# Kernel tuning notes

Measured on AMD Instinct MI355X. Metric: run time of the kernel, lower is better.

The kernel has to match this reference:

```python
import jax, jax.numpy as jnp
import numpy as np

H_IMG, W_IMG = 32, 32   # image_size -> seq_len = 1024
NH, HD, D = 8, 32, 256  # num_heads, head_dim, d_model
B = 8


def _relative_positions(h, w):
    # Swin-style relative position index table, [h*w, h*w] int32
    y = np.arange(h); x = np.arange(w)
    coords = np.stack(np.meshgrid(y, x, indexing='ij')).reshape(2, -1)  # [2, S]
    rel = coords[:, :, None] - coords[:, None, :]                      # [2, S, S]
    rel = rel.transpose(1, 2, 0).astype(np.int64)                      # [S, S, 2]
    rel[:, :, 0] += h - 1
    rel[:, :, 1] += w - 1
    rel[:, :, 0] *= 2 * w - 1
    return np.int32(rel.sum(-1))                                       # [S, S]

_POS = _relative_positions(H_IMG, W_IMG)


def setup_inputs() -> dict:
    key = jax.random.key(0)
    ks = jax.random.split(key, 8)
    S = H_IMG * W_IMG
    return {
        'inputs_q': jax.random.normal(ks[0], (B, S, D), jnp.float32),
        'inputs_kv': jax.random.normal(ks[1], (B, S, D), jnp.float32),
        'Wq': jax.random.normal(ks[2], (D, NH, HD), jnp.float32) / np.sqrt(D),
        'bq': jnp.zeros((NH, HD), jnp.float32),
        'Wk': jax.random.normal(ks[3], (D, NH, HD), jnp.float32) / np.sqrt(D),
        'bk': jnp.zeros((NH, HD), jnp.float32),
        'Wv': jax.random.normal(ks[4], (D, NH, HD), jnp.float32) / np.sqrt(D),
        'bv': jnp.zeros((NH, HD), jnp.float32),
        'rel_table': 0.02 * jax.random.normal(ks[5], ((2 * H_IMG - 1) * (2 * W_IMG - 1), NH), jnp.float32),
        'Wo': jax.random.normal(ks[6], (NH, HD, D), jnp.float32) / np.sqrt(NH * HD),
        'bo': jnp.zeros((D,), jnp.float32),
    }


def reference(inputs_q, inputs_kv, Wq, bq, Wk, bk, Wv, bv, rel_table, Wo, bo):
    pos = jnp.asarray(_POS)                                  # [S, S] int32 (constant)
    q = jnp.einsum('bsd,dhk->bshk', inputs_q, Wq) + bq       # [B, S, H, HD]
    k = jnp.einsum('bsd,dhk->bshk', inputs_kv, Wk) + bk
    v = jnp.einsum('bsd,dhk->bshk', inputs_kv, Wv) + bv
    q = q / jnp.sqrt(jnp.asarray(HD, q.dtype))
    attn = jnp.einsum('bqhd,bkhd->bhqk', q, k)               # [B, H, S, S]
    rel_bias = rel_table[pos]                                # [S, S, H]
    attn = attn + jnp.transpose(rel_bias, (2, 0, 1))[None]   # broadcast over batch
    attn = jax.nn.softmax(attn, axis=-1)
    x = jnp.einsum('bhqk,bkhd->bqhd', attn, v)               # [B, S, H, HD]
    return jnp.einsum('bqhd,hdf->bqf', x, Wo) + bo           # [B, S, D]
```

## Files before the change

kernel.cpp:

```cpp
#include <hip/hip_runtime.h>

#define B_SZ   8
#define S_LEN  1024
#define D_MOD  256
#define NHEADS 8
#define M_ROWS 8192
#define LOG2E  1.4426950408889634f
#define QSCALE_LOG2E 0.2550352766751165f

typedef _Float16 f16x8 __attribute__((ext_vector_type(8)));
typedef _Float16 f16x4 __attribute__((ext_vector_type(4)));
typedef float    f32x4 __attribute__((ext_vector_type(4)));

__global__ __launch_bounds__(256)
void prep_kernel(const float* __restrict__ Wq, const float* __restrict__ Wk,
                 const float* __restrict__ Wv, const float* __restrict__ Wo,
                 const float* __restrict__ rel,
                 _Float16* __restrict__ wtp, float* __restrict__ tab) {
    if (blockIdx.x < 32) {
        __shared__ _Float16 Wl[32 * 264];
        const int mi = blockIdx.x >> 3;
        const int k0 = (blockIdx.x & 7) << 5;
        const float* W = (mi == 0) ? Wq : (mi == 1) ? Wk : (mi == 2) ? Wv : Wo;
        {
            const int r  = threadIdx.x >> 3;
            const int c4 = (threadIdx.x & 7) * 4;
            const float* src = W + (size_t)(k0 + r) * 256 + c4;
#pragma unroll
            for (int g = 0; g < 8; ++g) {
                f32x4 v = *(const f32x4*)(src + g * 32);
                f16x4 o;
#pragma unroll
                for (int j = 0; j < 4; ++j) o[j] = (_Float16)v[j];
                *(f16x4*)(&Wl[r * 264 + c4 + g * 32]) = o;
            }
        }
        __syncthreads();
        const int n16 = threadIdx.x >> 4;
        const int l16 = threadIdx.x & 15;
        const int kk  = k0 >> 5;
#pragma unroll
        for (int quad = 0; quad < 4; ++quad) {
            f16x8 v;
#pragma unroll
            for (int j = 0; j < 8; ++j) v[j] = Wl[(quad * 8 + j) * 264 + n16 * 16 + l16];
            *(f16x8*)(wtp + (((size_t)(mi * 16 + n16) * 8 + kk) << 9) + (quad * 16 + l16) * 8) = v;
        }
        return;
    }
    __shared__ float rl[63 * 8];
    const int dy31 = blockIdx.x - 32;
    for (int f = threadIdx.x; f < 504; f += 256) rl[f] = rel[(size_t)dy31 * 504 + f];
    __syncthreads();
    const int h  = threadIdx.x >> 5;
    const int r5 = threadIdx.x & 31;
#pragma unroll
    for (int c = 0; c < 6; ++c) {
        const int oi   = r5 * 6 + c;
        const int e    = oi >> 6;
        const int lane = oi & 63;
        const int quad = lane >> 4, l16 = lane & 15;
        f32x4 v;
#pragma unroll
        for (int reg = 0; reg < 4; ++reg) {
            const int idx = 16 * e + l16 - quad * 4 - reg + 15;
            v[reg] = rl[idx * 8 + h] * LOG2E;
        }
        *(f32x4*)(tab + (((size_t)(h * 63 + dy31) * 3 + e) << 8) + lane * 4) = v;
    }
}

__global__ __launch_bounds__(256)
void gemm_qkv_kernel(const float* __restrict__ in_q, const float* __restrict__ in_kv,
                     const _Float16* __restrict__ wtp,
                     const float* __restrict__ bq, const float* __restrict__ bk,
                     const float* __restrict__ bv,
                     _Float16* __restrict__ qs, _Float16* __restrict__ ks,
                     _Float16* __restrict__ vs) {
    __shared__ __align__(16) _Float16 As[64 * 264];
    _Float16* Ta = As;
    _Float16* Tb = As + 64 * 72;

    const int tid  = threadIdx.x;
    const int w    = tid >> 6;
    const int lane = tid & 63;
    const int quad = lane >> 4;
    const int l16  = lane & 15;
    const int m0 = blockIdx.x * 64, n0 = blockIdx.y * 64, z = blockIdx.z;
    const int b = m0 >> 10, mloc = m0 & 1023;

    {
        const int r  = tid >> 2;
        const int c4 = (tid & 3) * 4;
        const float* src = (z ? in_kv : in_q) + (size_t)(m0 + r) * 256 + c4;
        _Float16* dst = As + r * 264 + c4;
#pragma unroll
        for (int g = 0; g < 16; ++g) {
            f32x4 v = *(const f32x4*)(src + g * 16);
            f16x4 o;
#pragma unroll
            for (int j = 0; j < 4; ++j) o[j] = (_Float16)v[j];
            *(f16x4*)(dst + g * 16) = o;
        }
    }
    __syncthreads();

    const int n16base = (n0 >> 4) + (w >> 1) * 2;
    const int mA = z ? 1 : 0;
    const _Float16* wA0 = wtp + (((size_t)(mA * 16 + n16base + 0) * 8) << 9) + lane * 8;
    const _Float16* wA1 = wtp + (((size_t)(mA * 16 + n16base + 1) * 8) << 9) + lane * 8;
    const _Float16* wV0 = wtp + (((size_t)(2 * 16 + n16base + 0) * 8) << 9) + lane * 8;
    const _Float16* wV1 = wtp + (((size_t)(2 * 16 + n16base + 1) * 8) << 9) + lane * 8;
    const _Float16* arow0 = As + ((w & 1) * 32 + l16) * 264;
    const _Float16* arow1 = arow0 + 16 * 264;

    f32x4 accA[2][2], accV[2][2];
#pragma unroll
    for (int i = 0; i < 2; ++i)
#pragma unroll
        for (int j = 0; j < 2; ++j) {
            accA[i][j] = (f32x4){0.f, 0.f, 0.f, 0.f};
            accV[i][j] = (f32x4){0.f, 0.f, 0.f, 0.f};
        }

#pragma unroll
    for (int kk = 0; kk < 8; ++kk) {
        const int k8 = kk * 32 + quad * 8;
        f16x8 a0 = *(const f16x8*)(arow0 + k8);
        f16x8 a1 = *(const f16x8*)(arow1 + k8);
        f16x8 w0 = *(const f16x8*)(wA0 + kk * 512);
        f16x8 w1 = *(const f16x8*)(wA1 + kk * 512);
        accA[0][0] = __builtin_amdgcn_mfma_f32_16x16x32_f16(w0, a0, accA[0][0], 0, 0, 0);
        accA[0][1] = __builtin_amdgcn_mfma_f32_16x16x32_f16(w0, a1, accA[0][1], 0, 0, 0);
        accA[1][0] = __builtin_amdgcn_mfma_f32_16x16x32_f16(w1, a0, accA[1][0], 0, 0, 0);
        accA[1][1] = __builtin_amdgcn_mfma_f32_16x16x32_f16(w1, a1, accA[1][1], 0, 0, 0);
        if (z == 1) {
            f16x8 v0 = *(const f16x8*)(wV0 + kk * 512);
            f16x8 v1 = *(const f16x8*)(wV1 + kk * 512);
            accV[0][0] = __builtin_amdgcn_mfma_f32_16x16x32_f16(a0, v0, accV[0][0], 0, 0, 0);
            accV[0][1] = __builtin_amdgcn_mfma_f32_16x16x32_f16(a0, v1, accV[0][1], 0, 0, 0);
            accV[1][0] = __builtin_amdgcn_mfma_f32_16x16x32_f16(a1, v0, accV[1][0], 0, 0, 0);
            accV[1][1] = __builtin_amdgcn_mfma_f32_16x16x32_f16(a1, v1, accV[1][1], 0, 0, 0);
        }
    }
    __syncthreads();

    {
        const float* biasA = z ? bk : bq;
        const float  sc    = z ? 1.0f : QSCALE_LOG2E;
#pragma unroll
        for (int i = 0; i < 2; ++i) {
            f32x4 b4 = *(const f32x4*)(biasA + n0 + (w >> 1) * 32 + i * 16 + quad * 4);
#pragma unroll
            for (int jj = 0; jj < 2; ++jj) {
                f16x4 pk;
#pragma unroll
                for (int r = 0; r < 4; ++r) pk[r] = (_Float16)((accA[i][jj][r] + b4[r]) * sc);
                *(f16x4*)(Ta + ((w & 1) * 32 + jj * 16 + l16) * 72 +
                               (w >> 1) * 32 + i * 16 + quad * 4) = pk;
            }
        }
        if (z == 1) {
#pragma unroll
            for (int i = 0; i < 2; ++i) {
                const float bvv = bv[n0 + (w >> 1) * 32 + i * 16 + l16];
#pragma unroll
                for (int jj = 0; jj < 2; ++jj) {
                    f16x4 pk;
#pragma unroll
                    for (int r = 0; r < 4; ++r) pk[r] = (_Float16)(accV[jj][i][r] + bvv);
                    *(f16x4*)(Tb + ((w >> 1) * 32 + i * 16 + l16) * 72 +
                                   (w & 1) * 32 + jj * 16 + quad * 4) = pk;
                }
            }
        }
    }
    __syncthreads();
    {
        const int l16c = tid & 15, qdc = (tid >> 4) & 3;
        const int tile0 = mloc >> 5;
#pragma unroll
        for (int c2i = 0; c2i < 2; ++c2i) {
            const int c2 = w * 2 + c2i;
            const int s2 = c2 >> 2, sub = (c2 >> 1) & 1, hs = c2 & 1;
            const int bh = b * 8 + (n0 >> 5) + hs;
            const size_t dbase = (((size_t)(bh * 32 + tile0 + s2) * 2 + sub) << 9) + lane * 8;
            f16x8 va = *(const f16x8*)(Ta + (s2 * 32 + sub * 16 + l16c) * 72 +
                                            hs * 32 + qdc * 8);
            *(f16x8*)((z ? ks : qs) + dbase) = va;
            if (z == 1) {
                f16x8 vb = *(const f16x8*)(Tb + (hs * 32 + sub * 16 + l16c) * 72 +
                                                s2 * 32 + qdc * 8);
                *(f16x8*)(vs + dbase) = vb;
            }
        }
    }
}

__global__ __launch_bounds__(256)
void gemm_out_kernel(const _Float16* __restrict__ xh, const _Float16* __restrict__ wtp,
                     const float* __restrict__ bo, float* __restrict__ out) {
    __shared__ __align__(16) _Float16 As[64 * 264];
    const int tid  = threadIdx.x;
    const int w    = tid >> 6;
    const int lane = tid & 63;
    const int quad = lane >> 4;
    const int l16  = lane & 15;
    const int m0 = blockIdx.x * 64, n0 = blockIdx.y * 64;

    {
        const int r  = tid >> 2;
        const int c8 = (tid & 3) * 8;
        const _Float16* src = xh + (size_t)(m0 + r) * 256 + c8;
        _Float16* dst = As + r * 264 + c8;
#pragma unroll
        for (int g = 0; g < 8; ++g)
            *(f16x8*)(dst + g * 32) = *(const f16x8*)(src + g * 32);
    }
    __syncthreads();

    const int n16base = 48 + (n0 >> 4) + (w >> 1) * 2;
    const _Float16* w0p = wtp + (((size_t)(n16base + 0) * 8) << 9) + lane * 8;
    const _Float16* w1p = wtp + (((size_t)(n16base + 1) * 8) << 9) + lane * 8;
    const _Float16* arow0 = As + ((w & 1) * 32 + l16) * 264;
    const _Float16* arow1 = arow0 + 16 * 264;

    f32x4 acc[2][2];
#pragma unroll
    for (int i = 0; i < 2; ++i)
#pragma unroll
        for (int j = 0; j < 2; ++j) acc[i][j] = (f32x4){0.f, 0.f, 0.f, 0.f};

#pragma unroll
    for (int kk = 0; kk < 8; ++kk) {
        const int k8 = kk * 32 + quad * 8;
        f16x8 a0 = *(const f16x8*)(arow0 + k8);
        f16x8 a1 = *(const f16x8*)(arow1 + k8);
        f16x8 b0 = *(const f16x8*)(w0p + kk * 512);
        f16x8 b1 = *(const f16x8*)(w1p + kk * 512);
        acc[0][0] = __builtin_amdgcn_mfma_f32_16x16x32_f16(a0, b0, acc[0][0], 0, 0, 0);
        acc[0][1] = __builtin_amdgcn_mfma_f32_16x16x32_f16(a0, b1, acc[0][1], 0, 0, 0);
        acc[1][0] = __builtin_amdgcn_mfma_f32_16x16x32_f16(a1, b0, acc[1][0], 0, 0, 0);
        acc[1][1] = __builtin_amdgcn_mfma_f32_16x16x32_f16(a1, b1, acc[1][1], 0, 0, 0);
    }

    __syncthreads();
    {
        float* Tf = (float*)As;
#pragma unroll
        for (int i = 0; i < 2; ++i) {
#pragma unroll
            for (int jj = 0; jj < 2; ++jj) {
#pragma unroll
                for (int r = 0; r < 4; ++r) {
                    const int row = (w & 1) * 32 + jj * 16 + quad * 4 + r;
                    const int col = (w >> 1) * 32 + i * 16 + l16;
                    Tf[row * 68 + col] = acc[jj][i][r];
                }
            }
        }
        __syncthreads();
        const f32x4 bv4 = *(const f32x4*)(bo + n0 + l16 * 4);
#pragma unroll
        for (int g = 0; g < 4; ++g) {
            const int row = w * 16 + g * 4 + quad;
            f32x4 v = *(const f32x4*)(Tf + row * 68 + l16 * 4);
            v += bv4;
            *(f32x4*)(out + (size_t)(m0 + row) * 256 + n0 + l16 * 4) = v;
        }
    }
}

__global__ __launch_bounds__(256)
void attn_kernel(const _Float16* __restrict__ qs, const _Float16* __restrict__ ks,
                 const _Float16* __restrict__ vs, const float* __restrict__ tab,
                 _Float16* __restrict__ xh) {
    __shared__ __align__(16) _Float16 Ps[4][32][40];

    const int tid  = threadIdx.x;
    const int w    = tid >> 6;
    const int lane = tid & 63;
    const int quad = lane >> 4;
    const int l16  = lane & 15;

    const int n     = blockIdx.x;
    const int xcd   = n & 7;
    const int local = n >> 3;
    const int bh    = xcd * 8 + (local & 7);
    const int qc    = local >> 3;
    const int b = bh >> 3, h = bh & 7;
    const int qrow_base = qc * 128 + w * 32;
    const int yq = qc * 4 + w;

    const _Float16* qp = qs + (((size_t)(bh * 32 + yq) * 2) << 9) + lane * 8;
    const f16x8 qf0 = *(const f16x8*)(qp);
    const f16x8 qf1 = *(const f16x8*)(qp + 512);
    const _Float16* kp = ks + (((size_t)bh * 64) << 9) + lane * 8;
    const _Float16* vp = vs + (((size_t)bh * 64) << 9) + lane * 8;
    const float* tb = tab + (((size_t)h * 63 * 3) << 8) + lane * 4;

    f16x8 ones;
#pragma unroll
    for (int j = 0; j < 8; ++j) ones[j] = (_Float16)1.0f;

    f32x4 o00 = {0.f,0.f,0.f,0.f}, o01 = {0.f,0.f,0.f,0.f};
    f32x4 o10 = {0.f,0.f,0.f,0.f}, o11 = {0.f,0.f,0.f,0.f};
    f32x4 ol0 = {0.f,0.f,0.f,0.f}, ol1 = {0.f,0.f,0.f,0.f};

    f16x8 kf0 = *(const f16x8*)(kp);
    f16x8 kf1 = *(const f16x8*)(kp + 512);
    f16x8 vf0 = *(const f16x8*)(vp);
    f16x8 vf1 = *(const f16x8*)(vp + 512);
    f32x4 c0 = *(const f32x4*)(tb + (yq + 31) * 768);
    f32x4 c1 = *(const f32x4*)(tb + (yq + 31) * 768 + 256);
    f32x4 c2 = *(const f32x4*)(tb + (yq + 31) * 768 + 512);

    for (int kt = 0; kt < 32; ++kt) {
        const bool more = (kt < 31);
        f16x8 nk0, nk1, nv0, nv1;
        f32x4 nc0, nc1, nc2;
        if (more) {
            const _Float16* kq = kp + (kt + 1) * 1024;
            nk0 = *(const f16x8*)(kq);
            nk1 = *(const f16x8*)(kq + 512);
            const _Float16* vq = vp + (kt + 1) * 1024;
            nv0 = *(const f16x8*)(vq);
            nv1 = *(const f16x8*)(vq + 512);
            const int d = (yq + 30 - kt) * 768;
            nc0 = *(const f32x4*)(tb + d);
            nc1 = *(const f32x4*)(tb + d + 256);
            nc2 = *(const f32x4*)(tb + d + 512);
        }

        __builtin_amdgcn_s_setprio(1);
        f32x4 s00 = __builtin_amdgcn_mfma_f32_16x16x32_f16(kf0, qf0, c1, 0, 0, 0);
        f32x4 s01 = __builtin_amdgcn_mfma_f32_16x16x32_f16(kf1, qf0, c0, 0, 0, 0);
        f32x4 s10 = __builtin_amdgcn_mfma_f32_16x16x32_f16(kf0, qf1, c2, 0, 0, 0);
        f32x4 s11 = __builtin_amdgcn_mfma_f32_16x16x32_f16(kf1, qf1, c1, 0, 0, 0);
        __builtin_amdgcn_s_setprio(0);

        f16x4 p;
#pragma unroll
        for (int r = 0; r < 4; ++r) p[r] = (_Float16)__builtin_amdgcn_exp2f(s00[r]);
        *(f16x4*)(&Ps[w][l16][quad * 4]) = p;
#pragma unroll
        for (int r = 0; r < 4; ++r) p[r] = (_Float16)__builtin_amdgcn_exp2f(s01[r]);
        *(f16x4*)(&Ps[w][l16][16 + quad * 4]) = p;
#pragma unroll
        for (int r = 0; r < 4; ++r) p[r] = (_Float16)__builtin_amdgcn_exp2f(s10[r]);
        *(f16x4*)(&Ps[w][16 + l16][quad * 4]) = p;
#pragma unroll
        for (int r = 0; r < 4; ++r) p[r] = (_Float16)__builtin_amdgcn_exp2f(s11[r]);
        *(f16x4*)(&Ps[w][16 + l16][16 + quad * 4]) = p;

        const f16x8 pf0 = *(const f16x8*)(&Ps[w][l16][quad * 8]);
        const f16x8 pf1 = *(const f16x8*)(&Ps[w][16 + l16][quad * 8]);
        __builtin_amdgcn_s_setprio(1);
        o00 = __builtin_amdgcn_mfma_f32_16x16x32_f16(vf0, pf0, o00, 0, 0, 0);
        o01 = __builtin_amdgcn_mfma_f32_16x16x32_f16(vf0, pf1, o01, 0, 0, 0);
        o10 = __builtin_amdgcn_mfma_f32_16x16x32_f16(vf1, pf0, o10, 0, 0, 0);
        o11 = __builtin_amdgcn_mfma_f32_16x16x32_f16(vf1, pf1, o11, 0, 0, 0);
        ol0 = __builtin_amdgcn_mfma_f32_16x16x32_f16(ones, pf0, ol0, 0, 0, 0);
        ol1 = __builtin_amdgcn_mfma_f32_16x16x32_f16(ones, pf1, ol1, 0, 0, 0);
        __builtin_amdgcn_s_setprio(0);

        if (more) {
            kf0 = nk0; kf1 = nk1; vf0 = nv0; vf1 = nv1;
            c0 = nc0; c1 = nc1; c2 = nc2;
        }
    }

#pragma unroll
    for (int qh = 0; qh < 2; ++qh) {
        const f32x4 onl = qh ? o01 : o00;
        const f32x4 onh = qh ? o11 : o10;
        const f32x4 ll  = qh ? ol1 : ol0;
        const float inv = __builtin_amdgcn_rcpf(ll[0]);
        const int qg = qrow_base + qh * 16 + l16;
        f16x4 u, v;
#pragma unroll
        for (int r = 0; r < 4; ++r) {
            u[r] = (_Float16)(onl[r] * inv);
            v[r] = (_Float16)(onh[r] * inv);
        }
        _Float16* op = xh + ((size_t)(b * S_LEN + qg)) * D_MOD + h * 32 + quad * 4;
        *(f16x4*)(op)      = u;
        *(f16x4*)(op + 16) = v;
    }
}

extern "C" void kernel_launch(void* const* d_in, const int* in_sizes, int n_in,
                              void* d_out, int out_size, void* d_ws, size_t ws_size,
                              hipStream_t stream) {
    const float* in_q  = (const float*)d_in[0];
    const float* in_kv = (const float*)d_in[1];
    const float* Wq    = (const float*)d_in[2];
    const float* bq    = (const float*)d_in[3];
    const float* Wk    = (const float*)d_in[4];
    const float* bk    = (const float*)d_in[5];
    const float* Wv    = (const float*)d_in[6];
    const float* bv    = (const float*)d_in[7];
    const float* rel   = (const float*)d_in[8];
    const float* Wo    = (const float*)d_in[9];
    const float* bo    = (const float*)d_in[10];
    float* out = (float*)d_out;

    char* wsb = (char*)d_ws;
    _Float16* qs  = (_Float16*)(wsb);
    _Float16* ks  = (_Float16*)(wsb + (size_t)4  * 1048576);
    _Float16* vs  = (_Float16*)(wsb + (size_t)8  * 1048576);
    _Float16* xh  = (_Float16*)(wsb + (size_t)12 * 1048576);
    _Float16* wtp = (_Float16*)(wsb + (size_t)16 * 1048576);
    float*    tab = (float*)   (wsb + (size_t)17 * 1048576);

    const dim3 blk(256);

    prep_kernel<<<dim3(95), blk, 0, stream>>>(Wq, Wk, Wv, Wo, rel, wtp, tab);
    gemm_qkv_kernel<<<dim3(128, 4, 2), blk, 0, stream>>>(
        in_q, in_kv, wtp, bq, bk, bv, qs, ks, vs);
    attn_kernel<<<dim3(512), blk, 0, stream>>>(qs, ks, vs, tab, xh);
    gemm_out_kernel<<<dim3(128, 4), blk, 0, stream>>>(xh, wtp, bo, out);
}
```

Measured before the change: 123.7 us.

## Share K/V tiles across waves via LDS double buffer and store bias table in fp16

Previously each of the four waves in the attention block loaded the full K and V tiles from global memory on its own. Now each wave loads one quarter of the K/V tile into a shared double buffer, and the block synchronises once per iteration before all waves read it, cutting global/L2 traffic by about 4x. The relative-position bias table is also stored as fp16 and widened to fp32 on load, which halves its bandwidth. The costs are a block-wide barrier every key tile, extra LDS reads and writes, and reduced precision in the bias term.

```diff
diff --git a/kernel.cpp b/kernel.cpp
--- a/kernel.cpp
+++ b/kernel.cpp
@@ -16,7 +16,7 @@
 void prep_kernel(const float* __restrict__ Wq, const float* __restrict__ Wk,
                  const float* __restrict__ Wv, const float* __restrict__ Wo,
                  const float* __restrict__ rel,
-                 _Float16* __restrict__ wtp, float* __restrict__ tab) {
+                 _Float16* __restrict__ wtp, _Float16* __restrict__ tab) {
     if (blockIdx.x < 32) {
         __shared__ _Float16 Wl[32 * 264];
         const int mi = blockIdx.x >> 3;
@@ -60,13 +60,13 @@
         const int e    = oi >> 6;
         const int lane = oi & 63;
         const int quad = lane >> 4, l16 = lane & 15;
-        f32x4 v;
+        f16x4 v;
 #pragma unroll
         for (int reg = 0; reg < 4; ++reg) {
             const int idx = 16 * e + l16 - quad * 4 - reg + 15;
-            v[reg] = rl[idx * 8 + h] * LOG2E;
-        }
-        *(f32x4*)(tab + (((size_t)(h * 63 + dy31) * 3 + e) << 8) + lane * 4) = v;
+            v[reg] = (_Float16)(rl[idx * 8 + h] * LOG2E);
+        }
+        *(f16x4*)(tab + (((size_t)(h * 63 + dy31) * 3 + e) << 8) + lane * 4) = v;
     }
 }
 
@@ -273,9 +273,10 @@
 
 __global__ __launch_bounds__(256)
 void attn_kernel(const _Float16* __restrict__ qs, const _Float16* __restrict__ ks,
-                 const _Float16* __restrict__ vs, const float* __restrict__ tab,
+                 const _Float16* __restrict__ vs, const _Float16* __restrict__ tab,
                  _Float16* __restrict__ xh) {
     __shared__ __align__(16) _Float16 Ps[4][32][40];
+    __shared__ __align__(16) _Float16 KVb[2][4][512];
 
     const int tid  = threadIdx.x;
     const int w    = tid >> 6;
@@ -295,9 +296,13 @@
     const _Float16* qp = qs + (((size_t)(bh * 32 + yq) * 2) << 9) + lane * 8;
     const f16x8 qf0 = *(const f16x8*)(qp);
     const f16x8 qf1 = *(const f16x8*)(qp + 512);
-    const _Float16* kp = ks + (((size_t)bh * 64) << 9) + lane * 8;
-    const _Float16* vp = vs + (((size_t)bh * 64) << 9) + lane * 8;
-    const float* tb = tab + (((size_t)h * 63 * 3) << 8) + lane * 4;
+
+    const _Float16* kv = ((w < 2) ? ks : vs) + (((size_t)bh * 64) << 9) +
+                         (w & 1) * 512 + lane * 8;
+    _Float16* myc0 = &KVb[0][w][lane * 8];
+    _Float16* myc1 = &KVb[1][w][lane * 8];
+
+    const _Float16* tb = tab + (((size_t)h * 189) << 8) + lane * 4;
 
     f16x8 ones;
 #pragma unroll
@@ -307,30 +312,37 @@
     f32x4 o10 = {0.f,0.f,0.f,0.f}, o11 = {0.f,0.f,0.f,0.f};
     f32x4 ol0 = {0.f,0.f,0.f,0.f}, ol1 = {0.f,0.f,0.f,0.f};
 
-    f16x8 kf0 = *(const f16x8*)(kp);
-    f16x8 kf1 = *(const f16x8*)(kp + 512);
-    f16x8 vf0 = *(const f16x8*)(vp);
-    f16x8 vf1 = *(const f16x8*)(vp + 512);
-    f32x4 c0 = *(const f32x4*)(tb + (yq + 31) * 768);
-    f32x4 c1 = *(const f32x4*)(tb + (yq + 31) * 768 + 256);
-    f32x4 c2 = *(const f32x4*)(tb + (yq + 31) * 768 + 512);
-
+    *(f16x8*)myc0 = *(const f16x8*)(kv);
+    f32x4 c0, c1, c2;
+    {
+        const _Float16* t = tb + (yq + 31) * 768;
+        f16x4 t0 = *(const f16x4*)(t);
+        f16x4 t1 = *(const f16x4*)(t + 256);
+        f16x4 t2 = *(const f16x4*)(t + 512);
+#pragma unroll
+        for (int r = 0; r < 4; ++r) {
+            c0[r] = (float)t0[r]; c1[r] = (float)t1[r]; c2[r] = (float)t2[r];
+        }
+    }
+    __syncthreads();
+
+    int cur = 0;
     for (int kt = 0; kt < 32; ++kt) {
         const bool more = (kt < 31);
-        f16x8 nk0, nk1, nv0, nv1;
-        f32x4 nc0, nc1, nc2;
+        f16x8 stg;
+        f16x4 n0, n1, n2;
         if (more) {
-            const _Float16* kq = kp + (kt + 1) * 1024;
-            nk0 = *(const f16x8*)(kq);
-            nk1 = *(const f16x8*)(kq + 512);
-            const _Float16* vq = vp + (kt + 1) * 1024;
-            nv0 = *(const f16x8*)(vq);
-            nv1 = *(const f16x8*)(vq + 512);
+            stg = *(const f16x8*)(kv + (kt + 1) * 1024);
             const int d = (yq + 30 - kt) * 768;
-            nc0 = *(const f32x4*)(tb + d);
-            nc1 = *(const f32x4*)(tb + d + 256);
-            nc2 = *(const f32x4*)(tb + d + 512);
-        }
+            n0 = *(const f16x4*)(tb + d);
+            n1 = *(const f16x4*)(tb + d + 256);
+            n2 = *(const f16x4*)(tb + d + 512);
+        }
+
+        const f16x8 kf0 = *(const f16x8*)(&KVb[cur][0][lane * 8]);
+        const f16x8 kf1 = *(const f16x8*)(&KVb[cur][1][lane * 8]);
+        const f16x8 vf0 = *(const f16x8*)(&KVb[cur][2][lane * 8]);
+        const f16x8 vf1 = *(const f16x8*)(&KVb[cur][3][lane * 8]);
 
         __builtin_amdgcn_s_setprio(1);
         f32x4 s00 = __builtin_amdgcn_mfma_f32_16x16x32_f16(kf0, qf0, c1, 0, 0, 0);
@@ -365,9 +377,14 @@
         __builtin_amdgcn_s_setprio(0);
 
         if (more) {
-            kf0 = nk0; kf1 = nk1; vf0 = nv0; vf1 = nv1;
-            c0 = nc0; c1 = nc1; c2 = nc2;
-        }
+            *(f16x8*)(cur ? myc0 : myc1) = stg;
+#pragma unroll
+            for (int r = 0; r < 4; ++r) {
+                c0[r] = (float)n0[r]; c1[r] = (float)n1[r]; c2[r] = (float)n2[r];
+            }
+        }
+        __syncthreads();
+        cur ^= 1;
     }
 
 #pragma unroll
@@ -411,7 +428,7 @@
     _Float16* vs  = (_Float16*)(wsb + (size_t)8  * 1048576);
     _Float16* xh  = (_Float16*)(wsb + (size_t)12 * 1048576);
     _Float16* wtp = (_Float16*)(wsb + (size_t)16 * 1048576);
-    float*    tab = (float*)   (wsb + (size_t)17 * 1048576);
+    _Float16* tab = (_Float16*)(wsb + (size_t)17 * 1048576);
 
     const dim3 blk(256);
 
```

Result: slower. 127.1 us (+2.7%).

## Halve per-wave tiles in attention and output GEMM to double grid parallelism

Applied to the files above, without the earlier changes.

The attention kernel now gives each wave 16 query rows instead of 32 and launches 1024 blocks instead of 512. The output GEMM block width drops from 64 to 32 columns and it launches 128x8 blocks. The relative-bias table is stored in fp16 to halve its loads, and launch bounds request 4 blocks per CU. The aim is more occupancy and latency hiding on a GPU with many CUs. The cost is that K/V fragments and the A tile are reloaded by twice as many blocks, and the bias loses precision.

```diff
diff --git a/kernel.cpp b/kernel.cpp
--- a/kernel.cpp
+++ b/kernel.cpp
@@ -16,7 +16,7 @@
 void prep_kernel(const float* __restrict__ Wq, const float* __restrict__ Wk,
                  const float* __restrict__ Wv, const float* __restrict__ Wo,
                  const float* __restrict__ rel,
-                 _Float16* __restrict__ wtp, float* __restrict__ tab) {
+                 _Float16* __restrict__ wtp, _Float16* __restrict__ tab) {
     if (blockIdx.x < 32) {
         __shared__ _Float16 Wl[32 * 264];
         const int mi = blockIdx.x >> 3;
@@ -60,13 +60,13 @@
         const int e    = oi >> 6;
         const int lane = oi & 63;
         const int quad = lane >> 4, l16 = lane & 15;
-        f32x4 v;
+        f16x4 v;
 #pragma unroll
         for (int reg = 0; reg < 4; ++reg) {
             const int idx = 16 * e + l16 - quad * 4 - reg + 15;
-            v[reg] = rl[idx * 8 + h] * LOG2E;
-        }
-        *(f32x4*)(tab + (((size_t)(h * 63 + dy31) * 3 + e) << 8) + lane * 4) = v;
+            v[reg] = (_Float16)(rl[idx * 8 + h] * LOG2E);
+        }
+        *(f16x4*)(tab + (((size_t)(h * 63 + dy31) * 3 + e) << 8) + lane * 4) = v;
     }
 }
 
@@ -197,7 +197,7 @@
     }
 }
 
-__global__ __launch_bounds__(256)
+__global__ __launch_bounds__(256, 4)
 void gemm_out_kernel(const _Float16* __restrict__ xh, const _Float16* __restrict__ wtp,
                      const float* __restrict__ bo, float* __restrict__ out) {
     __shared__ __align__(16) _Float16 As[64 * 264];
@@ -206,7 +206,7 @@
     const int lane = tid & 63;
     const int quad = lane >> 4;
     const int l16  = lane & 15;
-    const int m0 = blockIdx.x * 64, n0 = blockIdx.y * 64;
+    const int m0 = blockIdx.x * 64, n0 = blockIdx.y * 32;
 
     {
         const int r  = tid >> 2;
@@ -219,17 +219,12 @@
     }
     __syncthreads();
 
-    const int n16base = 48 + (n0 >> 4) + (w >> 1) * 2;
-    const _Float16* w0p = wtp + (((size_t)(n16base + 0) * 8) << 9) + lane * 8;
-    const _Float16* w1p = wtp + (((size_t)(n16base + 1) * 8) << 9) + lane * 8;
+    const int n16 = 48 + (n0 >> 4) + (w >> 1);
+    const _Float16* w0p = wtp + (((size_t)n16 * 8) << 9) + lane * 8;
     const _Float16* arow0 = As + ((w & 1) * 32 + l16) * 264;
     const _Float16* arow1 = arow0 + 16 * 264;
 
-    f32x4 acc[2][2];
-#pragma unroll
-    for (int i = 0; i < 2; ++i)
-#pragma unroll
-        for (int j = 0; j < 2; ++j) acc[i][j] = (f32x4){0.f, 0.f, 0.f, 0.f};
+    f32x4 acc0 = {0.f, 0.f, 0.f, 0.f}, acc1 = {0.f, 0.f, 0.f, 0.f};
 
 #pragma unroll
     for (int kk = 0; kk < 8; ++kk) {
@@ -237,45 +232,41 @@
         f16x8 a0 = *(const f16x8*)(arow0 + k8);
         f16x8 a1 = *(const f16x8*)(arow1 + k8);
         f16x8 b0 = *(const f16x8*)(w0p + kk * 512);
-        f16x8 b1 = *(const f16x8*)(w1p + kk * 512);
-        acc[0][0] = __builtin_amdgcn_mfma_f32_16x16x32_f16(a0, b0, acc[0][0], 0, 0, 0);
-        acc[0][1] = __builtin_amdgcn_mfma_f32_16x16x32_f16(a0, b1, acc[0][1], 0, 0, 0);
-        acc[1][0] = __builtin_amdgcn_mfma_f32_16x16x32_f16(a1, b0, acc[1][0], 0, 0, 0);
-        acc[1][1] = __builtin_amdgcn_mfma_f32_16x16x32_f16(a1, b1, acc[1][1], 0, 0, 0);
+        acc0 = __builtin_amdgcn_mfma_f32_16x16x32_f16(a0, b0, acc0, 0, 0, 0);
+        acc1 = __builtin_amdgcn_mfma_f32_16x16x32_f16(a1, b0, acc1, 0, 0, 0);
     }
 
     __syncthreads();
     {
         float* Tf = (float*)As;
-#pragma unroll
-        for (int i = 0; i < 2; ++i) {
-#pragma unroll
-            for (int jj = 0; jj < 2; ++jj) {
-#pragma unroll
-                for (int r = 0; r < 4; ++r) {
-                    const int row = (w & 1) * 32 + jj * 16 + quad * 4 + r;
-                    const int col = (w >> 1) * 32 + i * 16 + l16;
-                    Tf[row * 68 + col] = acc[jj][i][r];
-                }
+        const int col = (w >> 1) * 16 + l16;
+#pragma unroll
+        for (int jj = 0; jj < 2; ++jj) {
+            const f32x4 a = jj ? acc1 : acc0;
+#pragma unroll
+            for (int r = 0; r < 4; ++r) {
+                const int row = (w & 1) * 32 + jj * 16 + quad * 4 + r;
+                Tf[row * 36 + col] = a[r];
             }
         }
         __syncthreads();
-        const f32x4 bv4 = *(const f32x4*)(bo + n0 + l16 * 4);
-#pragma unroll
-        for (int g = 0; g < 4; ++g) {
-            const int row = w * 16 + g * 4 + quad;
-            f32x4 v = *(const f32x4*)(Tf + row * 68 + l16 * 4);
+        const int c4 = (tid & 7) * 4;
+        const f32x4 bv4 = *(const f32x4*)(bo + n0 + c4);
+#pragma unroll
+        for (int g = 0; g < 2; ++g) {
+            const int row = g * 32 + (tid >> 3);
+            f32x4 v = *(const f32x4*)(Tf + row * 36 + c4);
             v += bv4;
-            *(f32x4*)(out + (size_t)(m0 + row) * 256 + n0 + l16 * 4) = v;
+            *(f32x4*)(out + (size_t)(m0 + row) * 256 + n0 + c4) = v;
         }
     }
 }
 
-__global__ __launch_bounds__(256)
+__global__ __launch_bounds__(256, 4)
 void attn_kernel(const _Float16* __restrict__ qs, const _Float16* __restrict__ ks,
-                 const _Float16* __restrict__ vs, const float* __restrict__ tab,
+                 const _Float16* __restrict__ vs, const _Float16* __restrict__ tab,
                  _Float16* __restrict__ xh) {
-    __shared__ __align__(16) _Float16 Ps[4][32][40];
+    __shared__ __align__(16) _Float16 Ps[4][16][40];
 
     const int tid  = threadIdx.x;
     const int w    = tid >> 6;
@@ -289,36 +280,42 @@
     const int bh    = xcd * 8 + (local & 7);
     const int qc    = local >> 3;
     const int b = bh >> 3, h = bh & 7;
-    const int qrow_base = qc * 128 + w * 32;
-    const int yq = qc * 4 + w;
-
-    const _Float16* qp = qs + (((size_t)(bh * 32 + yq) * 2) << 9) + lane * 8;
-    const f16x8 qf0 = *(const f16x8*)(qp);
-    const f16x8 qf1 = *(const f16x8*)(qp + 512);
+    const int t16  = qc * 4 + w;
+    const int qsub = t16 & 1;
+    const int yq   = t16 >> 1;
+
+    const _Float16* qp = qs + (((size_t)(bh * 32 + (t16 >> 1)) * 2 + qsub) << 9) + lane * 8;
+    const f16x8 qf = *(const f16x8*)(qp);
+
     const _Float16* kp = ks + (((size_t)bh * 64) << 9) + lane * 8;
     const _Float16* vp = vs + (((size_t)bh * 64) << 9) + lane * 8;
-    const float* tb = tab + (((size_t)h * 63 * 3) << 8) + lane * 4;
+    const _Float16* tb = tab + (((size_t)h * 189) << 8) + lane * 4;
+    const int eA = (1 + qsub) << 8;
+    const int eB = qsub << 8;
 
     f16x8 ones;
 #pragma unroll
     for (int j = 0; j < 8; ++j) ones[j] = (_Float16)1.0f;
 
-    f32x4 o00 = {0.f,0.f,0.f,0.f}, o01 = {0.f,0.f,0.f,0.f};
-    f32x4 o10 = {0.f,0.f,0.f,0.f}, o11 = {0.f,0.f,0.f,0.f};
-    f32x4 ol0 = {0.f,0.f,0.f,0.f}, ol1 = {0.f,0.f,0.f,0.f};
+    f32x4 olo = {0.f,0.f,0.f,0.f}, ohi = {0.f,0.f,0.f,0.f}, osum = {0.f,0.f,0.f,0.f};
 
     f16x8 kf0 = *(const f16x8*)(kp);
     f16x8 kf1 = *(const f16x8*)(kp + 512);
     f16x8 vf0 = *(const f16x8*)(vp);
     f16x8 vf1 = *(const f16x8*)(vp + 512);
-    f32x4 c0 = *(const f32x4*)(tb + (yq + 31) * 768);
-    f32x4 c1 = *(const f32x4*)(tb + (yq + 31) * 768 + 256);
-    f32x4 c2 = *(const f32x4*)(tb + (yq + 31) * 768 + 512);
+    f32x4 cA, cB;
+    {
+        const int d = (yq + 31) * 768;
+        f16x4 tA = *(const f16x4*)(tb + d + eA);
+        f16x4 tB = *(const f16x4*)(tb + d + eB);
+#pragma unroll
+        for (int r = 0; r < 4; ++r) { cA[r] = (float)tA[r]; cB[r] = (float)tB[r]; }
+    }
 
     for (int kt = 0; kt < 32; ++kt) {
         const bool more = (kt < 31);
         f16x8 nk0, nk1, nv0, nv1;
-        f32x4 nc0, nc1, nc2;
+        f16x4 tA, tB;
         if (more) {
             const _Float16* kq = kp + (kt + 1) * 1024;
             nk0 = *(const f16x8*)(kq);
@@ -327,66 +324,48 @@
             nv0 = *(const f16x8*)(vq);
             nv1 = *(const f16x8*)(vq + 512);
             const int d = (yq + 30 - kt) * 768;
-            nc0 = *(const f32x4*)(tb + d);
-            nc1 = *(const f32x4*)(tb + d + 256);
-            nc2 = *(const f32x4*)(tb + d + 512);
+            tA = *(const f16x4*)(tb + d + eA);
+            tB = *(const f16x4*)(tb + d + eB);
         }
 
         __builtin_amdgcn_s_setprio(1);
-        f32x4 s00 = __builtin_amdgcn_mfma_f32_16x16x32_f16(kf0, qf0, c1, 0, 0, 0);
-        f32x4 s01 = __builtin_amdgcn_mfma_f32_16x16x32_f16(kf1, qf0, c0, 0, 0, 0);
-        f32x4 s10 = __builtin_amdgcn_mfma_f32_16x16x32_f16(kf0, qf1, c2, 0, 0, 0);
-        f32x4 s11 = __builtin_amdgcn_mfma_f32_16x16x32_f16(kf1, qf1, c1, 0, 0, 0);
+        f32x4 s0 = __builtin_amdgcn_mfma_f32_16x16x32_f16(kf0, qf, cA, 0, 0, 0);
+        f32x4 s1 = __builtin_amdgcn_mfma_f32_16x16x32_f16(kf1, qf, cB, 0, 0, 0);
         __builtin_amdgcn_s_setprio(0);
 
         f16x4 p;
 #pragma unroll
-        for (int r = 0; r < 4; ++r) p[r] = (_Float16)__builtin_amdgcn_exp2f(s00[r]);
+        for (int r = 0; r < 4; ++r) p[r] = (_Float16)__builtin_amdgcn_exp2f(s0[r]);
         *(f16x4*)(&Ps[w][l16][quad * 4]) = p;
 #pragma unroll
-        for (int r = 0; r < 4; ++r) p[r] = (_Float16)__builtin_amdgcn_exp2f(s01[r]);
+        for (int r = 0; r < 4; ++r) p[r] = (_Float16)__builtin_amdgcn_exp2f(s1[r]);
         *(f16x4*)(&Ps[w][l16][16 + quad * 4]) = p;
-#pragma unroll
-        for (int r = 0; r < 4; ++r) p[r] = (_Float16)__builtin_amdgcn_exp2f(s10[r]);
-        *(f16x4*)(&Ps[w][16 + l16][quad * 4]) = p;
-#pragma unroll
-        for (int r = 0; r < 4; ++r) p[r] = (_Float16)__builtin_amdgcn_exp2f(s11[r]);
-        *(f16x4*)(&Ps[w][16 + l16][16 + quad * 4]) = p;
-
-        const f16x8 pf0 = *(const f16x8*)(&Ps[w][l16][quad * 8]);
-        const f16x8 pf1 = *(const f16x8*)(&Ps[w][16 + l16][quad * 8]);
+
+        const f16x8 pf = *(const f16x8*)(&Ps[w][l16][quad * 8]);
         __builtin_amdgcn_s_setprio(1);
-        o00 = __builtin_amdgcn_mfma_f32_16x16x32_f16(vf0, pf0, o00, 0, 0, 0);
-        o01 = __builtin_amdgcn_mfma_f32_16x16x32_f16(vf0, pf1, o01, 0, 0, 0);
-        o10 = __builtin_amdgcn_mfma_f32_16x16x32_f16(vf1, pf0, o10, 0, 0, 0);
-        o11 = __builtin_amdgcn_mfma_f32_16x16x32_f16(vf1, pf1, o11, 0, 0, 0);
-        ol0 = __builtin_amdgcn_mfma_f32_16x16x32_f16(ones, pf0, ol0, 0, 0, 0);
-        ol1 = __builtin_amdgcn_mfma_f32_16x16x32_f16(ones, pf1, ol1, 0, 0, 0);
+        olo  = __builtin_amdgcn_mfma_f32_16x16x32_f16(vf0, pf, olo, 0, 0, 0);
+        ohi  = __builtin_amdgcn_mfma_f32_16x16x32_f16(vf1, pf, ohi, 0, 0, 0);
+        osum = __builtin_amdgcn_mfma_f32_16x16x32_f16(ones, pf, osum, 0, 0, 0);
         __builtin_amdgcn_s_setprio(0);
 
         if (more) {
             kf0 = nk0; kf1 = nk1; vf0 = nv0; vf1 = nv1;
-            c0 = nc0; c1 = nc1; c2 = nc2;
-        }
-    }
-
-#pragma unroll
-    for (int qh = 0; qh < 2; ++qh) {
-        const f32x4 onl = qh ? o01 : o00;
-        const f32x4 onh = qh ? o11 : o10;
-        const f32x4 ll  = qh ? ol1 : ol0;
-        const float inv = __builtin_amdgcn_rcpf(ll[0]);
-        const int qg = qrow_base + qh * 16 + l16;
-        f16x4 u, v;
-#pragma unroll
-        for (int r = 0; r < 4; ++r) {
-            u[r] = (_Float16)(onl[r] * inv);
-            v[r] = (_Float16)(onh[r] * inv);
-        }
-        _Float16* op = xh + ((size_t)(b * S_LEN + qg)) * D_MOD + h * 32 + quad * 4;
-        *(f16x4*)(op)      = u;
-        *(f16x4*)(op + 16) = v;
-    }
+#pragma unroll
+            for (int r = 0; r < 4; ++r) { cA[r] = (float)tA[r]; cB[r] = (float)tB[r]; }
+        }
+    }
+
+    const float inv = __builtin_amdgcn_rcpf(osum[0]);
+    const int qg = t16 * 16 + l16;
+    f16x4 u, v;
+#pragma unroll
+    for (int r = 0; r < 4; ++r) {
+        u[r] = (_Float16)(olo[r] * inv);
+        v[r] = (_Float16)(ohi[r] * inv);
+    }
+    _Float16* op = xh + ((size_t)(b * S_LEN + qg)) * D_MOD + h * 32 + quad * 4;
+    *(f16x4*)(op)      = u;
+    *(f16x4*)(op + 16) = v;
 }
 
 extern "C" void kernel_launch(void* const* d_in, const int* in_sizes, int n_in,
@@ -411,13 +390,13 @@
     _Float16* vs  = (_Float16*)(wsb + (size_t)8  * 1048576);
     _Float16* xh  = (_Float16*)(wsb + (size_t)12 * 1048576);
     _Float16* wtp = (_Float16*)(wsb + (size_t)16 * 1048576);
-    float*    tab = (float*)   (wsb + (size_t)17 * 1048576);
+    _Float16* tab = (_Float16*)(wsb + (size_t)17 * 1048576);
 
     const dim3 blk(256);
 
     prep_kernel<<<dim3(95), blk, 0, stream>>>(Wq, Wk, Wv, Wo, rel, wtp, tab);
     gemm_qkv_kernel<<<dim3(128, 4, 2), blk, 0, stream>>>(
         in_q, in_kv, wtp, bq, bk, bv, qs, ks, vs);
-    attn_kernel<<<dim3(512), blk, 0, stream>>>(qs, ks, vs, tab, xh);
-    gemm_out_kernel<<<dim3(128, 4), blk, 0, stream>>>(xh, wtp, bo, out);
+    attn_kernel<<<dim3(1024), blk, 0, stream>>>(qs, ks, vs, tab, xh);
+    gemm_out_kernel<<<dim3(128, 8), blk, 0, stream>>>(xh, wtp, bo, out);
 }
```

After: 129.0 us. 1.04x slower.
